# Kernel optimization log

Measured on AMD Instinct MI355X. Metric: run time of the kernel, lower is better.

Reference implementation:

```python
import jax, jax.numpy as jnp
import numpy as np

B, N, C = 8, 4096, 512
K = 512   # key_channels
V = 512   # value_channels (must equal in_channels for reprojection to typecheck)
H = 8     # head_count


def setup_inputs() -> dict:
    key = jax.random.key(0)
    ks = jax.random.split(key, 10)
    s = 1.0 / np.sqrt(C)
    return {
        "input_": jax.random.normal(ks[0], (B, N, C), jnp.float32),
        "y": jax.random.normal(ks[1], (B, N, C), jnp.float32),
        "Wk": jax.random.uniform(ks[2], (C, K), jnp.float32, -s, s),
        "bk": jax.random.uniform(ks[3], (K,), jnp.float32, -s, s),
        "Wq": jax.random.uniform(ks[4], (C, K), jnp.float32, -s, s),
        "bq": jax.random.uniform(ks[5], (K,), jnp.float32, -s, s),
        "Wv": jax.random.uniform(ks[6], (C, K), jnp.float32, -s, s),
        "bv": jax.random.uniform(ks[7], (K,), jnp.float32, -s, s),
        "Wr": jax.random.uniform(ks[8], (C, K), jnp.float32, -s, s),
        "br": jax.random.uniform(ks[9], (K,), jnp.float32, -s, s),
    }


def reference(input_, y, Wk, bk, Wq, bq, Wv, bv, Wr, br):
    hk = K // H  # head key channels
    hv = V // H  # head value channels
    # projections -> [B, N, H, h]
    keys = ((input_ + y) @ Wk + bk).reshape(B, N, H, hk)
    queries = (y @ Wq + bq).reshape(B, N, H, hk)
    values = (input_ @ Wv + bv).reshape(B, N, H, hv)
    # key softmax over tokens N; query softmax over head channels hk
    keys = jax.nn.softmax(keys, axis=1)
    queries = jax.nn.softmax(queries, axis=3)
    # context[b,h,k,v] = sum_n key[b,n,h,k] * value[b,n,h,v]
    context = jnp.einsum('bnhk,bnhv->bhkv', keys, values)
    # attended[b,n,h,v] = sum_k context[b,h,k,v] * query[b,n,h,k]
    attended = jnp.einsum('bhkv,bnhk->bnhv', context, queries)
    aggregated = attended.reshape(B, N, V)  # concat heads over value channels
    return aggregated @ Wr + br
```

## Files before the change

kernel.cpp:

```cpp
#include <hip/hip_runtime.h>
#include <hip/hip_bf16.h>
#include <stdint.h>


typedef __attribute__((ext_vector_type(8))) short short8;
typedef __attribute__((ext_vector_type(4))) float f32x4;
typedef __attribute__((ext_vector_type(4))) unsigned short us4;

__device__ __forceinline__ unsigned short f2bf(float f) {
  union { float f; unsigned u; } v; v.f = f;
  unsigned r = v.u + 0x7FFFu + ((v.u >> 16) & 1u);
  return (unsigned short)(r >> 16);
}
__device__ __forceinline__ float bf2f(unsigned short u) {
  union { unsigned u; float f; } v; v.u = ((unsigned)u) << 16;
  return v.f;
}
__device__ __forceinline__ ushort2 pk2(float a, float b) {
  __hip_bfloat162 h = __float22bfloat162_rn(float2{a, b});
  return *reinterpret_cast<ushort2*>(&h);
}
__device__ __forceinline__ us4 cvt4(float4 a) {
  ushort2 c0 = pk2(a.x, a.y), c1 = pk2(a.z, a.w);
  us4 r; r[0] = c0.x; r[1] = c0.y; r[2] = c1.x; r[3] = c1.y;
  return r;
}
__device__ __forceinline__ void gload16(const void* g, void* l) {
  __builtin_amdgcn_global_load_lds(
      (const __attribute__((address_space(1))) void*)g,
      (__attribute__((address_space(3))) void*)l, 16, 0, 0);
}

__global__ void prep_w(const float* __restrict__ Wk, const float* __restrict__ Wq,
                       const float* __restrict__ Wv, const float* __restrict__ Wr,
                       unsigned short* __restrict__ Wt, float* __restrict__ S) {
  __shared__ float tile[64][65];
  const int t = threadIdx.x;
  const int bx = blockIdx.x, by = blockIdx.y, w = blockIdx.z;
  if (w == 3 && bx == 0 && by == 0) {
#pragma unroll
    for (int i = 0; i < 16; ++i) S[i * 256 + t] = 0.f;
  }
  const float* W = (w == 0) ? Wk : (w == 1) ? Wq : (w == 2) ? Wv : Wr;
  unsigned short* O = Wt + (size_t)w * 512 * 512;
#pragma unroll
  for (int p = 0; p < 16; ++p) {
    int idx = p * 256 + t; int r = idx >> 6, c = idx & 63;
    tile[r][c] = W[(size_t)(by * 64 + r) * 512 + bx * 64 + c];
  }
  __syncthreads();
#pragma unroll
  for (int p = 0; p < 16; ++p) {
    int idx = p * 256 + t; int r = idx >> 6, c = idx & 63;
    O[(size_t)(bx * 64 + r) * 512 + by * 64 + c] = f2bf(tile[c][r]);
  }
}

__global__ __launch_bounds__(256) void prep_xy(const float* __restrict__ x, const float* __restrict__ y,
                        unsigned short* __restrict__ xb, unsigned short* __restrict__ yb,
                        unsigned short* __restrict__ xyb) {
  const size_t i = ((size_t)blockIdx.x * 256 + threadIdx.x) * 4;
  float4 a = *(const float4*)(x + i);
  float4 b = *(const float4*)(y + i);
  float4 s{a.x + b.x, a.y + b.y, a.z + b.z, a.w + b.w};
  *(us4*)(xb + i) = cvt4(a);
  *(us4*)(yb + i) = cvt4(b);
  *(us4*)(xyb + i) = cvt4(s);
}

template <int MODE>
__global__ __launch_bounds__(256) void gemm_bf16(const unsigned short* __restrict__ A,
                          const unsigned short* __restrict__ Bmat,
                          const float* __restrict__ bias, void* __restrict__ OutV,
                          float* __restrict__ S) {
  __shared__ __align__(16) unsigned short As[2][128][64];
  __shared__ __align__(16) unsigned short Bs[2][128][64];
  const int t = threadIdx.x, l = t & 63, w = t >> 6;
  const int lr = l & 15, lg = l >> 4;
  const int wr = w >> 1, wc = w & 1;
  const int bid = blockIdx.x;
  const int swz = (bid & 7) * 128 + (bid >> 3);
  const int tn = swz & 3, tm = swz >> 2;

  const unsigned short* Bbase = (MODE == 3) ? (Bmat + (size_t)(tm >> 5) * 262144) : Bmat;
  const int r0 = w * 8 + (l >> 3);
  const int su = ((l & 7) ^ (l >> 3)) * 8;
  const unsigned short* Ag = A + (size_t)(tm * 128 + r0) * 512 + su;
  const unsigned short* Bg = Bbase + (size_t)(tn * 128 + r0) * 512 + su;

  f32x4 acc[4][4] = {};

#define PSTAGE(buf, kt)                                                        \
  {                                                                            \
    _Pragma("unroll") for (int i = 0; i < 4; ++i) {                            \
      gload16(Ag + (size_t)i * 32 * 512 + (kt) * 64, &As[buf][i * 32 + w * 8][0]); \
      gload16(Bg + (size_t)i * 32 * 512 + (kt) * 64, &Bs[buf][i * 32 + w * 8][0]); \
    }                                                                          \
  }

  PSTAGE(0, 0)
  PSTAGE(1, 1)
  for (int kt = 0; kt < 8; ++kt) {
    const int cur = kt & 1;
    if (kt < 7) { asm volatile("s_waitcnt vmcnt(8)" ::: "memory"); }
    else        { asm volatile("s_waitcnt vmcnt(0)" ::: "memory"); }
    __builtin_amdgcn_s_barrier();
    asm volatile("" ::: "memory");
    __builtin_amdgcn_s_setprio(1);
#pragma unroll
    for (int kk = 0; kk < 2; ++kk) {
      short8 af[4], bf[4];
#pragma unroll
      for (int m = 0; m < 4; ++m)
        af[m] = *(const short8*)&As[cur][wr * 64 + m * 16 + lr][((kk * 4 + lg) ^ (lr & 7)) * 8];
#pragma unroll
      for (int n = 0; n < 4; ++n)
        bf[n] = *(const short8*)&Bs[cur][wc * 64 + n * 16 + lr][((kk * 4 + lg) ^ (lr & 7)) * 8];
#pragma unroll
      for (int m = 0; m < 4; ++m)
#pragma unroll
        for (int n = 0; n < 4; ++n)
          acc[m][n] = __builtin_amdgcn_mfma_f32_16x16x32_bf16(af[m], bf[n], acc[m][n], 0, 0, 0);
    }
    __builtin_amdgcn_s_setprio(0);
    asm volatile("" ::: "memory");
    __builtin_amdgcn_s_barrier();
    asm volatile("" ::: "memory");
    if (kt < 6) PSTAGE(cur, kt + 2)
  }
#undef PSTAGE

  const int c_base = tn * 128 + wc * 64;
  const int r_base = tm * 128 + wr * 64;
  float bv_[4];
#pragma unroll
  for (int n = 0; n < 4; ++n) bv_[n] = bias[c_base + n * 16 + lr];

  if (MODE == 1) {
    unsigned short* Out = (unsigned short*)OutV;
#pragma unroll
    for (int m = 0; m < 4; ++m) {
#pragma unroll
      for (int j = 0; j < 4; ++j) {
        float a0 = acc[m][0][j] + bv_[0], a1 = acc[m][1][j] + bv_[1];
        float a2 = acc[m][2][j] + bv_[2], a3 = acc[m][3][j] + bv_[3];
        float mx = fmaxf(fmaxf(a0, a1), fmaxf(a2, a3));
#pragma unroll
        for (int o = 1; o < 16; o <<= 1) mx = fmaxf(mx, __shfl_xor(mx, o));
        float e0 = __expf(a0 - mx), e1 = __expf(a1 - mx);
        float e2 = __expf(a2 - mx), e3 = __expf(a3 - mx);
        float s = e0 + e1 + e2 + e3;
#pragma unroll
        for (int o = 1; o < 16; o <<= 1) s += __shfl_xor(s, o);
        const float rs = 1.0f / s;
        const int row = r_base + m * 16 + lg * 4 + j;
        Out[(size_t)row * 512 + c_base + 0 * 16 + lr] = f2bf(e0 * rs);
        Out[(size_t)row * 512 + c_base + 1 * 16 + lr] = f2bf(e1 * rs);
        Out[(size_t)row * 512 + c_base + 2 * 16 + lr] = f2bf(e2 * rs);
        Out[(size_t)row * 512 + c_base + 3 * 16 + lr] = f2bf(e3 * rs);
      }
    }
  } else if (MODE == 3) {
    float* Out = (float*)OutV;
#pragma unroll
    for (int n = 0; n < 4; ++n) {
      const int col = c_base + n * 16 + lr;
#pragma unroll
      for (int m = 0; m < 4; ++m) {
        const int row = r_base + m * 16 + lg * 4;
#pragma unroll
        for (int j = 0; j < 4; ++j)
          Out[(size_t)(row + j) * 512 + col] = acc[m][n][j] + bv_[n];
      }
    }
  } else if (MODE == 0) {
    unsigned short* Out = (unsigned short*)OutV;
    const int b = (tm * 128) >> 12;
#pragma unroll
    for (int n = 0; n < 4; ++n) {
      const int col = c_base + n * 16 + lr;
      float srow = 0.f;
#pragma unroll
      for (int m = 0; m < 4; ++m) {
        const int row = r_base + m * 16 + lg * 4;
        const int nl = row & 4095;
        us4 v;
#pragma unroll
        for (int j = 0; j < 4; ++j) {
          float f = __expf(acc[m][n][j] + bv_[n]);
          srow += f;
          v[j] = f2bf(f);
        }
        *(us4*)&Out[((size_t)(b * 512 + col)) * 4096 + nl] = v;
      }
      srow += __shfl_xor(srow, 16);
      srow += __shfl_xor(srow, 32);
      if (lg == 0) atomicAdd(&S[b * 512 + col], srow);
    }
  } else {
    unsigned short* Out = (unsigned short*)OutV;
    const int b = (tm * 128) >> 12;
#pragma unroll
    for (int n = 0; n < 4; ++n) {
      const int col = c_base + n * 16 + lr;
#pragma unroll
      for (int m = 0; m < 4; ++m) {
        const int row = r_base + m * 16 + lg * 4;
        const int nl = row & 4095;
        us4 v;
#pragma unroll
        for (int j = 0; j < 4; ++j) v[j] = f2bf(acc[m][n][j] + bv_[n]);
        *(us4*)&Out[((size_t)(b * 512 + col)) * 4096 + nl] = v;
      }
    }
  }
}

__global__ void context_partial(const unsigned short* __restrict__ KeT,
                                const unsigned short* __restrict__ VT,
                                float* __restrict__ cp) {
  const int t = threadIdx.x, l = t & 63, w = t >> 6;
  const int lr = l & 15, lg = l >> 4;
  const int ch = blockIdx.x, h = blockIdx.y, b = blockIdx.z;
  const unsigned short* Kp = KeT + ((size_t)b * 512 + h * 64) * 4096;
  const unsigned short* Vp = VT + ((size_t)b * 512 + h * 64) * 4096;
  const int tok_w = ch * 1024 + w * 256;
  f32x4 acc[4][4] = {};
  for (int s = 0; s < 8; ++s) {
    const int tok = tok_w + s * 32 + lg * 8;
    short8 a[4], kf[4];
#pragma unroll
    for (int m = 0; m < 4; ++m) a[m] = *(const short8*)&Vp[(size_t)(m * 16 + lr) * 4096 + tok];
#pragma unroll
    for (int n = 0; n < 4; ++n) kf[n] = *(const short8*)&Kp[(size_t)(n * 16 + lr) * 4096 + tok];
#pragma unroll
    for (int m = 0; m < 4; ++m)
#pragma unroll
      for (int n = 0; n < 4; ++n)
        acc[m][n] = __builtin_amdgcn_mfma_f32_16x16x32_bf16(a[m], kf[n], acc[m][n], 0, 0, 0);
  }
  __shared__ float red[4][64][64];
#pragma unroll
  for (int m = 0; m < 4; ++m)
#pragma unroll
    for (int n = 0; n < 4; ++n)
#pragma unroll
      for (int j = 0; j < 4; ++j)
        red[w][m * 16 + lg * 4 + j][n * 16 + lr] = acc[m][n][j];
  __syncthreads();
  const int blk = (b * 8 + h) * 4 + ch;
  float* o = cp + (size_t)blk * 4096;
  for (int i = 0; i < 16; ++i) {
    int e = i * 256 + t;
    int v = e >> 6, k = e & 63;
    o[e] = red[0][v][k] + red[1][v][k] + red[2][v][k] + red[3][v][k];
  }
}

__global__ __launch_bounds__(256) void ctx_mm2(const float* __restrict__ cp,
                      const float* __restrict__ S, const unsigned short* __restrict__ Wrt,
                      unsigned short* __restrict__ MT) {
  __shared__ __align__(16) unsigned short ctx_lds[64][72];
  const int t = threadIdx.x, l = t & 63, w = t >> 6;
  const int lr = l & 15, lg = l >> 4;
  const int cc = blockIdx.x, h = blockIdx.y, b = blockIdx.z;
  const int bh = b * 8 + h;

  const int k = t & 63, vg = t >> 6;
  const float rs = 1.0f / S[bh * 64 + k];
  const float* pb = cp + (size_t)bh * 4 * 4096 + k;
#pragma unroll
  for (int half = 0; half < 2; ++half) {
    short8 pkv;
#pragma unroll
    for (int i = 0; i < 8; ++i) {
      const int v = vg * 16 + half * 8 + i;
      const size_t e = (size_t)v * 64;
      float vsum = pb[e] + pb[4096 + e] + pb[8192 + e] + pb[12288 + e];
      pkv[i] = (short)f2bf(vsum * rs);
    }
    *(short8*)&ctx_lds[k][vg * 16 + half * 8] = pkv;
  }
  __syncthreads();

  const int c0 = cc * 128 + w * 32;
  f32x4 acc[4][2] = {};
#pragma unroll
  for (int kk = 0; kk < 2; ++kk) {
    const int vb = kk * 32 + lg * 8;
    short8 a[4], bfr[2];
#pragma unroll
    for (int m = 0; m < 4; ++m) a[m] = *(const short8*)&ctx_lds[m * 16 + lr][vb];
#pragma unroll
    for (int n = 0; n < 2; ++n)
      bfr[n] = *(const short8*)&Wrt[(size_t)(c0 + n * 16 + lr) * 512 + h * 64 + vb];
#pragma unroll
    for (int m = 0; m < 4; ++m)
#pragma unroll
      for (int n = 0; n < 2; ++n)
        acc[m][n] = __builtin_amdgcn_mfma_f32_16x16x32_bf16(a[m], bfr[n], acc[m][n], 0, 0, 0);
  }
#pragma unroll
  for (int n = 0; n < 2; ++n) {
    const int c = c0 + n * 16 + lr;
#pragma unroll
    for (int m = 0; m < 4; ++m) {
      const int kq = m * 16 + lg * 4;
      us4 v;
#pragma unroll
      for (int j = 0; j < 4; ++j) v[j] = f2bf(acc[m][n][j]);
      *(us4*)&MT[((size_t)b * 512 + c) * 512 + h * 64 + kq] = v;
    }
  }
}

extern "C" void kernel_launch(void* const* d_in, const int* in_sizes, int n_in,
                              void* d_out, int out_size, void* d_ws, size_t ws_size,
                              hipStream_t stream) {
  (void)in_sizes; (void)n_in; (void)out_size; (void)ws_size;
  const float* x  = (const float*)d_in[0];
  const float* y  = (const float*)d_in[1];
  const float* Wk = (const float*)d_in[2];
  const float* bk = (const float*)d_in[3];
  const float* Wq = (const float*)d_in[4];
  const float* bq = (const float*)d_in[5];
  const float* Wv = (const float*)d_in[6];
  const float* bv = (const float*)d_in[7];
  const float* Wr = (const float*)d_in[8];
  const float* br = (const float*)d_in[9];
  float* out = (float*)d_out;

  char* ws = (char*)d_ws;
  unsigned short* Wt   = (unsigned short*)(ws + 0);
  unsigned short* xb   = (unsigned short*)(ws + 2097152);
  unsigned short* yb   = (unsigned short*)(ws + 35651584);
  unsigned short* xyb  = (unsigned short*)(ws + 69206016);
  unsigned short* KeT  = (unsigned short*)(ws + 102760448);
  unsigned short* VT   = (unsigned short*)(ws + 136314880);
  float* S             = (float*)(ws + 169869312);
  float* cp            = (float*)(ws + 169885696);
  unsigned short* MT   = (unsigned short*)(ws + 174080000);
  unsigned short* Qp   = xyb;

  prep_w<<<dim3(8, 8, 4), 256, 0, stream>>>(Wk, Wq, Wv, Wr, Wt, S);
  prep_xy<<<16384, 256, 0, stream>>>(x, y, xb, yb, xyb);
  gemm_bf16<0><<<1024, 256, 0, stream>>>(xyb, Wt, bk, KeT, S);
  gemm_bf16<2><<<1024, 256, 0, stream>>>(xb, Wt + 2 * 262144, bv, VT, nullptr);
  gemm_bf16<1><<<1024, 256, 0, stream>>>(yb, Wt + 262144, bq, Qp, nullptr);
  context_partial<<<dim3(4, 8, 8), 256, 0, stream>>>(KeT, VT, cp);
  ctx_mm2<<<dim3(4, 8, 8), 256, 0, stream>>>(cp, S, Wt + 3 * 262144, MT);
  gemm_bf16<3><<<1024, 256, 0, stream>>>(Qp, MT, br, out, nullptr);
}
```

Measured before the change: 186.5 us.

## Interleave bf16 x, y, x+y rows and run the query GEMM right before reprojection

The three bf16 copies of the activations now sit in one row-interleaved buffer with a 1536-element stride, and the GEMM kernel takes an A stride parameter. The query projection moves to just before the final reprojection and writes into the KeT buffer, which context_partial has already finished reading. The aim is better cache locality and L2 reuse of the freshly written query output by the last GEMM. The risk is that each GEMM now reads with a strided pattern and only uses a third of every row it loads, which can hurt DRAM efficiency.

```diff
diff --git a/kernel.cpp b/kernel.cpp
--- a/kernel.cpp
+++ b/kernel.cpp
@@ -57,19 +57,22 @@
 }
 
 __global__ __launch_bounds__(256) void prep_xy(const float* __restrict__ x, const float* __restrict__ y,
-                        unsigned short* __restrict__ xb, unsigned short* __restrict__ yb,
-                        unsigned short* __restrict__ xyb) {
-  const size_t i = ((size_t)blockIdx.x * 256 + threadIdx.x) * 4;
-  float4 a = *(const float4*)(x + i);
-  float4 b = *(const float4*)(y + i);
+                        unsigned short* __restrict__ L) {
+  const size_t flat = ((size_t)blockIdx.x * 256 + threadIdx.x) * 4;
+  const size_t row = flat >> 9;
+  const int col = (int)(flat & 511);
+  float4 a = *(const float4*)(x + flat);
+  float4 b = *(const float4*)(y + flat);
   float4 s{a.x + b.x, a.y + b.y, a.z + b.z, a.w + b.w};
-  *(us4*)(xb + i) = cvt4(a);
-  *(us4*)(yb + i) = cvt4(b);
-  *(us4*)(xyb + i) = cvt4(s);
+  unsigned short* Lr = L + row * 1536;
+  *(us4*)(Lr + col) = cvt4(a);
+  *(us4*)(Lr + 512 + col) = cvt4(b);
+  *(us4*)(Lr + 1024 + col) = cvt4(s);
 }
 
 template <int MODE>
 __global__ __launch_bounds__(256) void gemm_bf16(const unsigned short* __restrict__ A,
+                          int astride,
                           const unsigned short* __restrict__ Bmat,
                           const float* __restrict__ bias, void* __restrict__ OutV,
                           float* __restrict__ S) {
@@ -85,15 +88,16 @@
   const unsigned short* Bbase = (MODE == 3) ? (Bmat + (size_t)(tm >> 5) * 262144) : Bmat;
   const int r0 = w * 8 + (l >> 3);
   const int su = ((l & 7) ^ (l >> 3)) * 8;
-  const unsigned short* Ag = A + (size_t)(tm * 128 + r0) * 512 + su;
+  const unsigned short* Ag = A + (size_t)(tm * 128 + r0) * astride + su;
   const unsigned short* Bg = Bbase + (size_t)(tn * 128 + r0) * 512 + su;
+  const size_t a32 = (size_t)32 * astride;
 
   f32x4 acc[4][4] = {};
 
 #define PSTAGE(buf, kt)                                                        \
   {                                                                            \
     _Pragma("unroll") for (int i = 0; i < 4; ++i) {                            \
-      gload16(Ag + (size_t)i * 32 * 512 + (kt) * 64, &As[buf][i * 32 + w * 8][0]); \
+      gload16(Ag + a32 * i + (kt) * 64, &As[buf][i * 32 + w * 8][0]);          \
       gload16(Bg + (size_t)i * 32 * 512 + (kt) * 64, &Bs[buf][i * 32 + w * 8][0]); \
     }                                                                          \
   }
@@ -332,22 +336,20 @@
 
   char* ws = (char*)d_ws;
   unsigned short* Wt   = (unsigned short*)(ws + 0);
-  unsigned short* xb   = (unsigned short*)(ws + 2097152);
-  unsigned short* yb   = (unsigned short*)(ws + 35651584);
-  unsigned short* xyb  = (unsigned short*)(ws + 69206016);
+  unsigned short* L    = (unsigned short*)(ws + 2097152);
   unsigned short* KeT  = (unsigned short*)(ws + 102760448);
   unsigned short* VT   = (unsigned short*)(ws + 136314880);
   float* S             = (float*)(ws + 169869312);
   float* cp            = (float*)(ws + 169885696);
   unsigned short* MT   = (unsigned short*)(ws + 174080000);
-  unsigned short* Qp   = xyb;
+  unsigned short* Qp   = KeT;
 
   prep_w<<<dim3(8, 8, 4), 256, 0, stream>>>(Wk, Wq, Wv, Wr, Wt, S);
-  prep_xy<<<16384, 256, 0, stream>>>(x, y, xb, yb, xyb);
-  gemm_bf16<0><<<1024, 256, 0, stream>>>(xyb, Wt, bk, KeT, S);
-  gemm_bf16<2><<<1024, 256, 0, stream>>>(xb, Wt + 2 * 262144, bv, VT, nullptr);
-  gemm_bf16<1><<<1024, 256, 0, stream>>>(yb, Wt + 262144, bq, Qp, nullptr);
+  prep_xy<<<16384, 256, 0, stream>>>(x, y, L);
+  gemm_bf16<0><<<1024, 256, 0, stream>>>(L + 1024, 1536, Wt, bk, KeT, S);
+  gemm_bf16<2><<<1024, 256, 0, stream>>>(L, 1536, Wt + 2 * 262144, bv, VT, nullptr);
   context_partial<<<dim3(4, 8, 8), 256, 0, stream>>>(KeT, VT, cp);
   ctx_mm2<<<dim3(4, 8, 8), 256, 0, stream>>>(cp, S, Wt + 3 * 262144, MT);
-  gemm_bf16<3><<<1024, 256, 0, stream>>>(Qp, MT, br, out, nullptr);
-}
+  gemm_bf16<1><<<1024, 256, 0, stream>>>(L + 512, 1536, Wt + 262144, bq, Qp, nullptr);
+  gemm_bf16<3><<<1024, 256, 0, stream>>>(Qp, 512, MT, br, out, nullptr);
+}
```

New measurement: 192.7 us. 3.3% more time.

## Replace value-projection GEMM with 256x256-tile triple-buffered MFMA kernel

Applied to the files above, without the earlier changes.

Adds a dedicated value-projection GEMM using 256x256 output tiles, 512-thread blocks, a swizzled three-stage LDS ring fed by asynchronous global-to-LDS loads, and raised priority around the MFMA bursts. It replaces the generic 128-tile gemm_bf16 MODE 2 launch, whose epilogue branch is removed. The larger tiles are meant to cut redundant operand loads and overlap loads with compute. In exchange, only 256 blocks are launched with heavy register and LDS use, so occupancy is lower and the tail effects differ.

```diff
diff --git a/kernel.cpp b/kernel.cpp
--- a/kernel.cpp
+++ b/kernel.cpp
@@ -173,7 +173,7 @@
           Out[(size_t)(row + j) * 512 + col] = acc[m][n][j] + bv_[n];
       }
     }
-  } else if (MODE == 0) {
+  } else {
     unsigned short* Out = (unsigned short*)OutV;
     const int b = (tm * 128) >> 12;
 #pragma unroll
@@ -197,21 +197,97 @@
       srow += __shfl_xor(srow, 32);
       if (lg == 0) atomicAdd(&S[b * 512 + col], srow);
     }
-  } else {
-    unsigned short* Out = (unsigned short*)OutV;
-    const int b = (tm * 128) >> 12;
-#pragma unroll
-    for (int n = 0; n < 4; ++n) {
-      const int col = c_base + n * 16 + lr;
-#pragma unroll
-      for (int m = 0; m < 4; ++m) {
-        const int row = r_base + m * 16 + lg * 4;
-        const int nl = row & 4095;
-        us4 v;
-#pragma unroll
-        for (int j = 0; j < 4; ++j) v[j] = f2bf(acc[m][n][j] + bv_[n]);
-        *(us4*)&Out[((size_t)(b * 512 + col)) * 4096 + nl] = v;
+  }
+}
+
+__global__ __launch_bounds__(512) void gemm_v256(const unsigned short* __restrict__ A,
+                          const unsigned short* __restrict__ Bt,
+                          const float* __restrict__ bias,
+                          unsigned short* __restrict__ Out) {
+  __shared__ __align__(16) unsigned short lds[3][4][64][64];
+  const int t = threadIdx.x, l = t & 63, w = t >> 6;
+  const int lr = l & 15, lg = l >> 4;
+  const int wr = w >> 2, wc = w & 3;
+  const int bid = blockIdx.x;
+  const int swz = (bid & 7) * 32 + (bid >> 3);
+  const int tn = swz & 1, tm = swz >> 1;
+
+  const int swu = (t & 7) ^ ((t >> 3) & 7);
+  const int row_g = 2 * (t >> 3) + (swu >> 2);
+  const int col8 = (swu & 3) * 8;
+  const unsigned short* Asrc = A + (size_t)(tm * 256 + row_g) * 512 + col8;
+  const unsigned short* Bsrc = Bt + (size_t)(tn * 256 + row_g) * 512 + col8;
+
+  const int rhalf = lr >> 1;
+  const int fu = (((lr & 1) * 4 + lg) ^ rhalf) * 8;
+
+  f32x4 acc[8][4] = {};
+
+#define VSTAGE(blk, kt, buf)                                                   \
+  {                                                                            \
+    const unsigned short* s_ =                                                 \
+        (((blk) < 2) ? (Asrc + (size_t)(blk) * 128 * 512)                      \
+                     : (Bsrc + (size_t)((blk) - 2) * 128 * 512)) + (kt) * 32;  \
+    gload16(s_, &lds[buf][blk][w * 8][0]);                                     \
+  }
+
+  VSTAGE(0, 0, 0) VSTAGE(1, 0, 0) VSTAGE(2, 0, 0) VSTAGE(3, 0, 0)
+  VSTAGE(0, 1, 1) VSTAGE(1, 1, 1) VSTAGE(2, 1, 1) VSTAGE(3, 1, 1)
+  asm volatile("s_waitcnt vmcnt(4)" ::: "memory");
+  __builtin_amdgcn_s_barrier();
+  asm volatile("" ::: "memory");
+
+  for (int it = 0; it < 16; ++it) {
+    const int cur = it % 3, stb = (it + 2) % 3;
+    const int ktn = it + 2;
+#pragma unroll
+    for (int q = 0; q < 4; ++q) {
+      const int mh = q >> 1, nh = q & 1;
+      short8 af[4], bf[2];
+#pragma unroll
+      for (int mp = 0; mp < 4; ++mp)
+        af[mp] = *(const short8*)&lds[cur][wr][(mh * 4 + mp) * 8 + rhalf][fu];
+#pragma unroll
+      for (int np = 0; np < 2; ++np)
+        bf[np] = *(const short8*)&lds[cur][2 + (wc >> 1)][(wc & 1) * 32 + (nh * 2 + np) * 8 + rhalf][fu];
+      if (it < 14) VSTAGE(q, ktn, stb)
+      __builtin_amdgcn_s_setprio(1);
+#pragma unroll
+      for (int mp = 0; mp < 4; ++mp)
+#pragma unroll
+        for (int np = 0; np < 2; ++np)
+          acc[mh * 4 + mp][nh * 2 + np] = __builtin_amdgcn_mfma_f32_16x16x32_bf16(
+              af[mp], bf[np], acc[mh * 4 + mp][nh * 2 + np], 0, 0, 0);
+      __builtin_amdgcn_s_setprio(0);
+      asm volatile("" ::: "memory");
+      if (q == 3) {
+        if (it < 14) { asm volatile("s_waitcnt vmcnt(4)" ::: "memory"); }
+        else         { asm volatile("s_waitcnt vmcnt(0)" ::: "memory"); }
       }
+      __builtin_amdgcn_s_barrier();
+      asm volatile("" ::: "memory");
+    }
+  }
+#undef VSTAGE
+
+  asm volatile("s_waitcnt vmcnt(0) lgkmcnt(0)" ::: "memory");
+  const int c_base = tn * 256 + wc * 64;
+  const int r_base = tm * 256 + wr * 128;
+  const int b = r_base >> 12;
+  float bv_[4];
+#pragma unroll
+  for (int n = 0; n < 4; ++n) bv_[n] = bias[c_base + n * 16 + lr];
+#pragma unroll
+  for (int n = 0; n < 4; ++n) {
+    const int col = c_base + n * 16 + lr;
+#pragma unroll
+    for (int m = 0; m < 8; ++m) {
+      const int row = r_base + m * 16 + lg * 4;
+      const int nl = row & 4095;
+      us4 v;
+#pragma unroll
+      for (int j = 0; j < 4; ++j) v[j] = f2bf(acc[m][n][j] + bv_[n]);
+      *(us4*)&Out[((size_t)(b * 512 + col)) * 4096 + nl] = v;
     }
   }
 }
@@ -345,7 +421,7 @@
   prep_w<<<dim3(8, 8, 4), 256, 0, stream>>>(Wk, Wq, Wv, Wr, Wt, S);
   prep_xy<<<16384, 256, 0, stream>>>(x, y, xb, yb, xyb);
   gemm_bf16<0><<<1024, 256, 0, stream>>>(xyb, Wt, bk, KeT, S);
-  gemm_bf16<2><<<1024, 256, 0, stream>>>(xb, Wt + 2 * 262144, bv, VT, nullptr);
+  gemm_v256<<<256, 512, 0, stream>>>(xb, Wt + 2 * 262144, bv, VT);
   gemm_bf16<1><<<1024, 256, 0, stream>>>(yb, Wt + 262144, bq, Qp, nullptr);
   context_partial<<<dim3(4, 8, 8), 256, 0, stream>>>(KeT, VT, cp);
   ctx_mm2<<<dim3(4, 8, 8), 256, 0, stream>>>(cp, S, Wt + 3 * 262144, MT);
```

After: 182.8 us (median of 2 runs). 1.02x faster.
